# Optimization experiments

Hardware: AMD Instinct MI355X
Metric: run time of the kernel (lower is better)

## Reference

```python
import jax, jax.numpy as jnp
import numpy as np

EMBED_DIM = 1024
NUM_HEADS = 16
HEAD_DIM = EMBED_DIM // NUM_HEADS


def setup_inputs() -> dict:
    key = jax.random.key(0)
    ks = jax.random.split(key, 6)
    B, S, D = 2, 2048, EMBED_DIM
    scale = 1.0 / np.sqrt(D)
    return {
        "inputs": jax.random.normal(ks[0], (B, S, D), dtype=jnp.float32),
        "Wq": jax.random.normal(ks[1], (D, D), dtype=jnp.float32) * scale,
        "Wk": jax.random.normal(ks[2], (D, D), dtype=jnp.float32) * scale,
        "Wv": jax.random.normal(ks[3], (D, D), dtype=jnp.float32) * scale,
        "Wo": jax.random.normal(ks[4], (D, D), dtype=jnp.float32) * scale,
        "bo": jnp.zeros((D,), dtype=jnp.float32),
    }


def reference(inputs, Wq, Wk, Wv, Wo, bo):
    B, S, D = inputs.shape
    H, P = NUM_HEADS, HEAD_DIM
    # torch Linear: x @ W.T ; weights stored [out, in]
    q = inputs @ Wq.T
    k = inputs @ Wk.T
    v = inputs @ Wv.T
    # separate heads: [B, S, H, P] -> [B, H, S, P]
    q = q.reshape(B, S, H, P).transpose(0, 2, 1, 3)
    k = k.reshape(B, S, H, P).transpose(0, 2, 1, 3)
    v = v.reshape(B, S, H, P).transpose(0, 2, 1, 3)
    # scaled dot-product attention; scale = 1/sqrt(P + 1e-9)
    scale = 1.0 / jnp.sqrt(jnp.float32(P) + 1e-9)
    scores = jnp.einsum("bhsp,bhtp->bhst", q, k) * scale
    weights = jax.nn.softmax(scores, axis=-1)
    attn = jnp.einsum("bhst,bhtp->bhsp", weights, v)
    # merge heads -> [B, S, D]
    concat = attn.transpose(0, 2, 1, 3).reshape(B, S, D)
    return concat @ Wo.T + bo
```

## Files before the change

kernel.cpp:

```cpp
#include <hip/hip_runtime.h>
#include <hip/hip_bf16.h>

typedef __bf16 bf16;
typedef __bf16 bf16x4 __attribute__((ext_vector_type(4)));
typedef __bf16 bf16x8 __attribute__((ext_vector_type(8)));
typedef short  s16x4  __attribute__((ext_vector_type(4)));
typedef float  f32x4  __attribute__((ext_vector_type(4)));

#define QSCALE 0.18033688011112042f

__device__ __forceinline__ void load16_lds(const bf16* g, bf16* l) {
    __builtin_amdgcn_global_load_lds(
        (const __attribute__((address_space(1))) unsigned int*)g,
        (__attribute__((address_space(3))) unsigned int*)l, 16, 0, 0);
}

__global__ void cvt_f32_bf16(
    const float* __restrict__ s0, const float* __restrict__ s1,
    const float* __restrict__ s2, const float* __restrict__ s3,
    const float* __restrict__ s4,
    bf16* __restrict__ d0, bf16* __restrict__ d1, bf16* __restrict__ d2,
    bf16* __restrict__ d3, bf16* __restrict__ d4)
{
    const float* s; bf16* d; int nblk;
    switch (blockIdx.y) {
        case 0:  s = s0; d = d0; nblk = 2048; break;
        case 1:  s = s1; d = d1; nblk = 512;  break;
        case 2:  s = s2; d = d2; nblk = 512;  break;
        case 3:  s = s3; d = d3; nblk = 512;  break;
        default: s = s4; d = d4; nblk = 512;  break;
    }
    if ((int)blockIdx.x >= nblk) return;
    int idx = blockIdx.x * 256 + threadIdx.x;
    float4 a = ((const float4*)s)[idx * 2];
    float4 b = ((const float4*)s)[idx * 2 + 1];
    bf16x8 o;
    o[0] = (bf16)a.x; o[1] = (bf16)a.y; o[2] = (bf16)a.z; o[3] = (bf16)a.w;
    o[4] = (bf16)b.x; o[5] = (bf16)b.y; o[6] = (bf16)b.z; o[7] = (bf16)b.w;
    *(bf16x8*)&d[idx * 8] = o;
}

__global__ __launch_bounds__(256, 2) void qkv_gemm(
    const bf16* __restrict__ A,
    const bf16* __restrict__ Wq, const bf16* __restrict__ Wk,
    const bf16* __restrict__ Wv,
    bf16* __restrict__ qbuf, bf16* __restrict__ kbuf, bf16* __restrict__ vT)
{
    __shared__ bf16 sA[128 * 32];
    __shared__ bf16 sB[128 * 32];

    const int which = blockIdx.x >> 3;
    const int n0    = (blockIdx.x & 7) * 128;
    const int m0    = blockIdx.y * 128;
    const bf16* B   = (which == 0) ? Wq : (which == 1) ? Wk : Wv;

    const int tid  = threadIdx.x;
    const int lane = tid & 63;
    const int w    = tid >> 6;
    const int wr   = w >> 1, wc = w & 1;
    const int r    = lane & 15;
    const int qd   = lane >> 4;

    f32x4 acc[4][4];
    const f32x4 zero4 = {0.f, 0.f, 0.f, 0.f};
#pragma unroll
    for (int mi = 0; mi < 4; ++mi)
#pragma unroll
        for (int ni = 0; ni < 4; ++ni) acc[mi][ni] = zero4;

    for (int kt = 0; kt < 32; ++kt) {
        const bf16* gA = A + (size_t)m0 * 1024 + kt * 32;
        const bf16* gB = B + (size_t)n0 * 1024 + kt * 32;
        __syncthreads();
#pragma unroll
        for (int j = 0; j < 2; ++j) {
            int task = j * 256 + tid;
            int row  = task >> 2, ch = task & 3;
            int ldsb = (j * 256 + w * 64) * 8;
            load16_lds(gA + (size_t)row * 1024 + ch * 8, &sA[ldsb]);
            load16_lds(gB + (size_t)row * 1024 + ch * 8, &sB[ldsb]);
        }
        __syncthreads();

        bf16x8 af[4], bfr[4];
#pragma unroll
        for (int mi = 0; mi < 4; ++mi)
            af[mi] = *(const bf16x8*)&sA[(wr * 64 + mi * 16 + r) * 32 + qd * 8];
#pragma unroll
        for (int ni = 0; ni < 4; ++ni)
            bfr[ni] = *(const bf16x8*)&sB[(wc * 64 + ni * 16 + r) * 32 + qd * 8];
#pragma unroll
        for (int mi = 0; mi < 4; ++mi)
#pragma unroll
            for (int ni = 0; ni < 4; ++ni)
                acc[mi][ni] = __builtin_amdgcn_mfma_f32_16x16x32_bf16(
                    af[mi], bfr[ni], acc[mi][ni], 0, 0, 0);
    }

    const float scale = (which == 0) ? QSCALE : 1.0f;
#pragma unroll
    for (int mi = 0; mi < 4; ++mi)
#pragma unroll
        for (int ni = 0; ni < 4; ++ni)
#pragma unroll
            for (int i = 0; i < 4; ++i) {
                int row = m0 + wr * 64 + mi * 16 + qd * 4 + i;
                int col = n0 + wc * 64 + ni * 16 + r;
                float v = acc[mi][ni][i] * scale;
                if (which == 0) {
                    qbuf[(size_t)row * 1024 + col] = (bf16)v;
                } else if (which == 1) {
                    kbuf[(size_t)row * 1024 + col] = (bf16)v;
                } else {
                    vT[((size_t)((row >> 11) * 1024 + col)) * 2048 + (row & 2047)] = (bf16)v;
                }
            }
}

__global__ __launch_bounds__(256, 2) void out_gemm(
    const bf16* __restrict__ A, const bf16* __restrict__ B,
    float* __restrict__ C, const float* __restrict__ bias)
{
    __shared__ bf16 sA[128 * 32];
    __shared__ bf16 sB[64 * 32];

    const int tid  = threadIdx.x;
    const int lane = tid & 63;
    const int w    = tid >> 6;
    const int wr   = w >> 1, wc = w & 1;
    const int r    = lane & 15;
    const int qd   = lane >> 4;
    const int m0   = blockIdx.y * 128;
    const int n0   = blockIdx.x * 64;

    f32x4 acc[4][2];
    const f32x4 zero4 = {0.f, 0.f, 0.f, 0.f};
#pragma unroll
    for (int mi = 0; mi < 4; ++mi)
#pragma unroll
        for (int ni = 0; ni < 2; ++ni) acc[mi][ni] = zero4;

    for (int kt = 0; kt < 32; ++kt) {
        const bf16* gA = A + (size_t)m0 * 1024 + kt * 32;
        const bf16* gB = B + (size_t)n0 * 1024 + kt * 32;
        __syncthreads();
#pragma unroll
        for (int j = 0; j < 2; ++j) {
            int task = j * 256 + tid;
            int row  = task >> 2, ch = task & 3;
            int ldsb = (j * 256 + w * 64) * 8;
            load16_lds(gA + (size_t)row * 1024 + ch * 8, &sA[ldsb]);
        }
        {
            int row = tid >> 2, ch = tid & 3;
            int ldsb = (w * 64) * 8;
            load16_lds(gB + (size_t)row * 1024 + ch * 8, &sB[ldsb]);
        }
        __syncthreads();

        bf16x8 af[4], bfr[2];
#pragma unroll
        for (int mi = 0; mi < 4; ++mi)
            af[mi] = *(const bf16x8*)&sA[(wr * 64 + mi * 16 + r) * 32 + qd * 8];
#pragma unroll
        for (int ni = 0; ni < 2; ++ni)
            bfr[ni] = *(const bf16x8*)&sB[(wc * 32 + ni * 16 + r) * 32 + qd * 8];
#pragma unroll
        for (int mi = 0; mi < 4; ++mi)
#pragma unroll
            for (int ni = 0; ni < 2; ++ni)
                acc[mi][ni] = __builtin_amdgcn_mfma_f32_16x16x32_bf16(
                    af[mi], bfr[ni], acc[mi][ni], 0, 0, 0);
    }

#pragma unroll
    for (int mi = 0; mi < 4; ++mi)
#pragma unroll
        for (int ni = 0; ni < 2; ++ni)
#pragma unroll
            for (int i = 0; i < 4; ++i) {
                int row = m0 + wr * 64 + mi * 16 + qd * 4 + i;
                int col = n0 + wc * 32 + ni * 16 + r;
                C[(size_t)row * 1024 + col] = acc[mi][ni][i] + bias[col];
            }
}

__global__ __launch_bounds__(256, 2) void attn_kernel(
    const bf16* __restrict__ qbuf, const bf16* __restrict__ kbuf,
    const bf16* __restrict__ vT, bf16* __restrict__ concat)
{
    __shared__ bf16 smem[2 * 64 * 72];
    bf16* sK = smem;
    bf16* sV = smem + 64 * 72;

    const int tid  = threadIdx.x;
    const int lane = tid & 63;
    const int w    = tid >> 6;
    const int r    = lane & 15;
    const int qd   = lane >> 4;
    const int qt   = blockIdx.x;
    const int bh   = blockIdx.y;
    const int b    = bh >> 4, h = bh & 15;
    const int qrow0 = b * 2048 + qt * 128;
    const size_t vbase = (size_t)bh * 64 * 2048;

    const s16x4 ones4 = {(short)0x3F80, (short)0x3F80, (short)0x3F80, (short)0x3F80};

    bf16x8 aq[2][2];
#pragma unroll
    for (int mi = 0; mi < 2; ++mi)
#pragma unroll
        for (int ks = 0; ks < 2; ++ks)
            aq[mi][ks] = *(const bf16x8*)&qbuf[
                (size_t)(qrow0 + w * 32 + mi * 16 + r) * 1024 + h * 64 + ks * 32 + qd * 8];

    f32x4 acc_o[2][4], acc_l[2];
    const f32x4 zero4 = {0.f, 0.f, 0.f, 0.f};
#pragma unroll
    for (int mi = 0; mi < 2; ++mi) {
        acc_l[mi] = zero4;
#pragma unroll
        for (int pj = 0; pj < 4; ++pj) acc_o[mi][pj] = zero4;
    }

    for (int tt = 0; tt < 32; ++tt) {
        bf16x8 rk[2], rv[2];
        int krow[2], kch[2];
#pragma unroll
        for (int t = 0; t < 2; ++t) {
            int flat = t * 256 + tid;
            krow[t] = flat >> 3; kch[t] = flat & 7;
            rk[t] = *(const bf16x8*)&kbuf[(size_t)(b * 2048 + tt * 64 + krow[t]) * 1024 + h * 64 + kch[t] * 8];
            rv[t] = *(const bf16x8*)&vT[vbase + (size_t)krow[t] * 2048 + tt * 64 + kch[t] * 8];
        }
        __syncthreads();
#pragma unroll
        for (int t = 0; t < 2; ++t) {
            *(bf16x8*)&sK[krow[t] * 72 + kch[t] * 8] = rk[t];
            *(bf16x8*)&sV[krow[t] * 72 + kch[t] * 8] = rv[t];
        }
        __syncthreads();

        f32x4 accs[2][4];
#pragma unroll
        for (int mi = 0; mi < 2; ++mi)
#pragma unroll
            for (int ni = 0; ni < 4; ++ni) accs[mi][ni] = zero4;
#pragma unroll
        for (int ks = 0; ks < 2; ++ks)
#pragma unroll
            for (int ni = 0; ni < 4; ++ni) {
                bf16x8 ak = *(const bf16x8*)&sK[(ni * 16 + r) * 72 + ks * 32 + qd * 8];
#pragma unroll
                for (int mi = 0; mi < 2; ++mi)
                    accs[mi][ni] = __builtin_amdgcn_mfma_f32_16x16x32_bf16(
                        ak, aq[mi][ks], accs[mi][ni], 0, 0, 0);
            }

        s16x4 pfrag[2][4];
#pragma unroll
        for (int mi = 0; mi < 2; ++mi)
#pragma unroll
            for (int ni = 0; ni < 4; ++ni) {
                bf16x4 pv;
#pragma unroll
                for (int i = 0; i < 4; ++i) pv[i] = (bf16)exp2f(accs[mi][ni][i]);
                pfrag[mi][ni] = __builtin_bit_cast(s16x4, pv);
            }

#pragma unroll
        for (int ni = 0; ni < 4; ++ni) {
#pragma unroll
            for (int pj = 0; pj < 4; ++pj) {
                bf16x4 av = *(const bf16x4*)&sV[(pj * 16 + r) * 72 + ni * 16 + qd * 4];
                s16x4  avs = __builtin_bit_cast(s16x4, av);
#pragma unroll
                for (int mi = 0; mi < 2; ++mi)
                    acc_o[mi][pj] = __builtin_amdgcn_mfma_f32_16x16x16bf16_1k(
                        avs, pfrag[mi][ni], acc_o[mi][pj], 0, 0, 0);
            }
#pragma unroll
            for (int mi = 0; mi < 2; ++mi)
                acc_l[mi] = __builtin_amdgcn_mfma_f32_16x16x16bf16_1k(
                    ones4, pfrag[mi][ni], acc_l[mi], 0, 0, 0);
        }
    }

    __syncthreads();
    bf16* scratch = smem;
#pragma unroll
    for (int mi = 0; mi < 2; ++mi) {
        float inv = 1.0f / acc_l[mi][0];
        int qloc  = w * 32 + mi * 16 + r;
#pragma unroll
        for (int pj = 0; pj < 4; ++pj)
#pragma unroll
            for (int i = 0; i < 4; ++i)
                scratch[qloc * 64 + pj * 16 + qd * 4 + i] =
                    (bf16)(acc_o[mi][pj][i] * inv);
    }
    __syncthreads();
    {
        int row  = tid >> 1;
        int half = tid & 1;
#pragma unroll
        for (int c = 0; c < 4; ++c) {
            bf16x8 v = *(const bf16x8*)&scratch[row * 64 + half * 32 + c * 8];
            *(bf16x8*)&concat[(size_t)(qrow0 + row) * 1024 + h * 64 + half * 32 + c * 8] = v;
        }
    }
}

extern "C" void kernel_launch(void* const* d_in, const int* in_sizes, int n_in,
                              void* d_out, int out_size, void* d_ws, size_t ws_size,
                              hipStream_t stream)
{
    const float* x  = (const float*)d_in[0];
    const float* Wq = (const float*)d_in[1];
    const float* Wk = (const float*)d_in[2];
    const float* Wv = (const float*)d_in[3];
    const float* Wo = (const float*)d_in[4];
    const float* bo = (const float*)d_in[5];
    float* out = (float*)d_out;

    char* ws = (char*)d_ws;
    bf16* xb     = (bf16*)(ws);
    bf16* Wqb    = (bf16*)(ws + (8u  << 20));
    bf16* Wkb    = (bf16*)(ws + (10u << 20));
    bf16* Wvb    = (bf16*)(ws + (12u << 20));
    bf16* Wob    = (bf16*)(ws + (14u << 20));
    bf16* qbuf   = (bf16*)(ws + (16u << 20));
    bf16* kbuf   = (bf16*)(ws + (24u << 20));
    bf16* vT     = (bf16*)(ws + (32u << 20));
    bf16* concat = (bf16*)(ws + (40u << 20));

    hipLaunchKernelGGL(cvt_f32_bf16, dim3(2048, 5), dim3(256), 0, stream,
                       x, Wq, Wk, Wv, Wo, xb, Wqb, Wkb, Wvb, Wob);
    hipLaunchKernelGGL(qkv_gemm, dim3(24, 32), dim3(256), 0, stream,
                       xb, Wqb, Wkb, Wvb, qbuf, kbuf, vT);
    hipLaunchKernelGGL(attn_kernel, dim3(16, 32), dim3(256), 0, stream,
                       qbuf, kbuf, vT, concat);
    hipLaunchKernelGGL(out_gemm, dim3(16, 32), dim3(256), 0, stream,
                       concat, Wob, out, bo);
}
```

Baseline: 215.8 us.

## Double-buffer K/V tiles in LDS with register prefetch two tiles ahead

The attention kernel now keeps two LDS stages for the K and V tiles. Each iteration stores the already-prefetched next tile into the spare stage and issues the global loads for the tile after that, then computes on the current stage. This cuts the two barriers per iteration to one and hides global load latency behind the MFMA work. In exchange LDS use doubles to about 36 KB per block, register pressure rises, and the last iteration reloads one redundant tile.

```diff
diff --git a/kernel.cpp b/kernel.cpp
--- a/kernel.cpp
+++ b/kernel.cpp
@@ -189,9 +189,7 @@
     const bf16* __restrict__ qbuf, const bf16* __restrict__ kbuf,
     const bf16* __restrict__ vT, bf16* __restrict__ concat)
 {
-    __shared__ bf16 smem[2 * 64 * 72];
-    bf16* sK = smem;
-    bf16* sV = smem + 64 * 72;
+    __shared__ bf16 sKV[4 * 64 * 72];
 
     const int tid  = threadIdx.x;
     const int lane = tid & 63;
@@ -206,6 +204,13 @@
 
     const s16x4 ones4 = {(short)0x3F80, (short)0x3F80, (short)0x3F80, (short)0x3F80};
 
+    int krow[2], kch[2];
+#pragma unroll
+    for (int t = 0; t < 2; ++t) {
+        int flat = t * 256 + tid;
+        krow[t] = flat >> 3; kch[t] = flat & 7;
+    }
+
     bf16x8 aq[2][2];
 #pragma unroll
     for (int mi = 0; mi < 2; ++mi)
@@ -223,23 +228,43 @@
         for (int pj = 0; pj < 4; ++pj) acc_o[mi][pj] = zero4;
     }
 
+    bf16x8 rk[2], rv[2];
+#pragma unroll
+    for (int t = 0; t < 2; ++t) {
+        rk[t] = *(const bf16x8*)&kbuf[(size_t)(b * 2048 + krow[t]) * 1024 + h * 64 + kch[t] * 8];
+        rv[t] = *(const bf16x8*)&vT[vbase + (size_t)krow[t] * 2048 + kch[t] * 8];
+    }
+#pragma unroll
+    for (int t = 0; t < 2; ++t) {
+        *(bf16x8*)&sKV[0 * 4608 + krow[t] * 72 + kch[t] * 8] = rk[t];
+        *(bf16x8*)&sKV[1 * 4608 + krow[t] * 72 + kch[t] * 8] = rv[t];
+    }
+#pragma unroll
+    for (int t = 0; t < 2; ++t) {
+        rk[t] = *(const bf16x8*)&kbuf[(size_t)(b * 2048 + 64 + krow[t]) * 1024 + h * 64 + kch[t] * 8];
+        rv[t] = *(const bf16x8*)&vT[vbase + (size_t)krow[t] * 2048 + 64 + kch[t] * 8];
+    }
+    __syncthreads();
+
     for (int tt = 0; tt < 32; ++tt) {
-        bf16x8 rk[2], rv[2];
-        int krow[2], kch[2];
-#pragma unroll
-        for (int t = 0; t < 2; ++t) {
-            int flat = t * 256 + tid;
-            krow[t] = flat >> 3; kch[t] = flat & 7;
-            rk[t] = *(const bf16x8*)&kbuf[(size_t)(b * 2048 + tt * 64 + krow[t]) * 1024 + h * 64 + kch[t] * 8];
-            rv[t] = *(const bf16x8*)&vT[vbase + (size_t)krow[t] * 2048 + tt * 64 + kch[t] * 8];
-        }
-        __syncthreads();
-#pragma unroll
-        for (int t = 0; t < 2; ++t) {
-            *(bf16x8*)&sK[krow[t] * 72 + kch[t] * 8] = rk[t];
-            *(bf16x8*)&sV[krow[t] * 72 + kch[t] * 8] = rv[t];
-        }
-        __syncthreads();
+        {
+            int st = (tt + 1) & 1;
+#pragma unroll
+            for (int t = 0; t < 2; ++t) {
+                *(bf16x8*)&sKV[(2 * st + 0) * 4608 + krow[t] * 72 + kch[t] * 8] = rk[t];
+                *(bf16x8*)&sKV[(2 * st + 1) * 4608 + krow[t] * 72 + kch[t] * 8] = rv[t];
+            }
+        }
+        {
+            int nxt = (tt + 2 < 32) ? tt + 2 : 31;
+#pragma unroll
+            for (int t = 0; t < 2; ++t) {
+                rk[t] = *(const bf16x8*)&kbuf[(size_t)(b * 2048 + nxt * 64 + krow[t]) * 1024 + h * 64 + kch[t] * 8];
+                rv[t] = *(const bf16x8*)&vT[vbase + (size_t)krow[t] * 2048 + nxt * 64 + kch[t] * 8];
+            }
+        }
+        const bf16* sK = &sKV[(2 * (tt & 1) + 0) * 4608];
+        const bf16* sV = &sKV[(2 * (tt & 1) + 1) * 4608];
 
         f32x4 accs[2][4];
 #pragma unroll
@@ -284,10 +309,11 @@
                 acc_l[mi] = __builtin_amdgcn_mfma_f32_16x16x16bf16_1k(
                     ones4, pfrag[mi][ni], acc_l[mi], 0, 0, 0);
         }
-    }
-
-    __syncthreads();
-    bf16* scratch = smem;
+
+        __syncthreads();
+    }
+
+    bf16* scratch = sKV;
 #pragma unroll
     for (int mi = 0; mi < 2; ++mi) {
         float inv = 1.0f / acc_l[mi][0];
@@ -296,7 +322,7 @@
         for (int pj = 0; pj < 4; ++pj)
 #pragma unroll
             for (int i = 0; i < 4; ++i)
-                scratch[qloc * 64 + pj * 16 + qd * 4 + i] =
+                scratch[qloc * 72 + pj * 16 + qd * 4 + i] =
                     (bf16)(acc_o[mi][pj][i] * inv);
     }
     __syncthreads();
@@ -305,7 +331,7 @@
         int half = tid & 1;
 #pragma unroll
         for (int c = 0; c < 4; ++c) {
-            bf16x8 v = *(const bf16x8*)&scratch[row * 64 + half * 32 + c * 8];
+            bf16x8 v = *(const bf16x8*)&scratch[row * 72 + half * 32 + c * 8];
             *(bf16x8*)&concat[(size_t)(qrow0 + row) * 1024 + h * 64 + half * 32 + c * 8] = v;
         }
     }
```

Result: faster. 205.0 us (-5.0%).
